# Performance work log

Measured on AMD Instinct MI355X. Metric: run time of the kernel, lower is better.

Reference implementation:

```python
import jax, jax.numpy as jnp
import numpy as np

N = 1024            # codeword length (power of 2)
NS = 10             # log2(N) butterfly stages
NUM_ITER = 10       # BP iterations
LLR_MAX = 19.3      # internal LLR clipping value
BS = 512            # batch size
FROZEN_POS = np.arange(64)
INFO_POS = np.setdiff1d(np.arange(N), FROZEN_POS)
K = len(INFO_POS)   # 960 information bits

# Precompute the per-stage butterfly gather patterns (static numpy indices).
_ind_range = np.arange(N // 2)
IND_1 = [(_ind_range * 2 - np.mod(_ind_range, 2 ** s)) for s in range(NS)]
IND_2 = [IND_1[s] + 2 ** s for s in range(NS)]
IND_INV = [np.argsort(np.concatenate([IND_1[s], IND_2[s]])) for s in range(NS)]


def _boxplus(x, y):
    # check-node update, matches tf: log(1+exp(x+y)) - log(exp(x)+exp(y))
    x = jnp.clip(x, -LLR_MAX, LLR_MAX)
    y = jnp.clip(y, -LLR_MAX, LLR_MAX)
    return jnp.log(1.0 + jnp.exp(x + y)) - jnp.log(jnp.exp(x) + jnp.exp(y))


def _bp_forward(llr_in):
    llr_ch = -llr_in  # logits -> internal llr sign convention (as in sionna's call)
    bs = llr_ch.shape[0]
    # a-priori right-messages: LLR_MAX at frozen positions, 0 elsewhere
    msg_r_in = jnp.zeros((1, N), jnp.float32).at[:, FROZEN_POS].set(LLR_MAX)
    msg_r_in = jnp.broadcast_to(msg_r_in, (bs, N))

    def one_iter(msg_l_prev, _):
        # msg_l_prev: [NS+1, bs, N]; slot s+1 feeds stage s of the next r-pass.
        # Initialized to zeros, which reproduces the ind_it==0 zero-init branch.
        # ---- right-going (check-node) pass, stages 0..NS-1 ----
        r_msgs = [msg_r_in]  # slot 0
        for s in range(NS):
            l_in = llr_ch if s == NS - 1 else msg_l_prev[s + 1]
            l1, l2 = l_in[:, IND_1[s]], l_in[:, IND_2[s]]
            r_in = r_msgs[s]
            r1, r2 = r_in[:, IND_1[s]], r_in[:, IND_2[s]]
            r1_out = _boxplus(r1, l2 + r2)
            r2_out = _boxplus(r1, l1) + r2
            r_out = jnp.concatenate([r1_out, r2_out], axis=1)[:, IND_INV[s]]
            r_msgs.append(r_out)
        # ---- left-going (bit-node) pass, stages NS-1..0 ----
        l_msgs = [None] * (NS + 1)
        l_msgs[NS] = llr_ch
        for s in range(NS - 1, -1, -1):
            l_in = l_msgs[s + 1]
            l1, l2 = l_in[:, IND_1[s]], l_in[:, IND_2[s]]
            r_in = r_msgs[s]
            r1, r2 = r_in[:, IND_1[s]], r_in[:, IND_2[s]]
            l1_out = _boxplus(l1, l2 + r2)
            l2_out = _boxplus(r1, l1) + l2
            l_msgs[s] = jnp.concatenate([l1_out, l2_out], axis=1)[:, IND_INV[s]]
        return jnp.stack(l_msgs, axis=0), None

    msg_l0 = jnp.zeros((NS + 1, bs, N), jnp.float32)
    msg_l, _ = jax.lax.scan(one_iter, msg_l0, None, length=NUM_ITER)
    u_hat = msg_l[0][:, INFO_POS]  # [bs, k] soft estimates (internal llr domain)
    return -u_hat                   # flip back to input logit convention


def setup_inputs() -> dict:
    key = jax.random.key(0)
    llr_ch = 2.0 * jax.random.normal(key, (BS, N), dtype=jnp.float32)
    return {"llr_ch": llr_ch}


def reference(llr_ch):
    return _bp_forward(llr_ch)
```

## Files before the change

### kernel.cpp

```cpp
#include <hip/hip_runtime.h>

#define BSZ 512
#define KOUT 960
#define EMAX 2.4092698e8f
#define EMIN 4.1506346e-9f

__device__ __forceinline__ float boxpE(float ex, float ey) {
    ex = fminf(fmaxf(ex, EMIN), EMAX);
    ey = fminf(fmaxf(ey, EMIN), EMAX);
    float num = __builtin_fmaf(ex, ey, 1.0f);
    float den = ex + ey;
    return num * __builtin_amdgcn_rcpf(den);
}

__global__ __launch_bounds__(512, 4) void polar_bp(const float* __restrict__ in,
                                                   float* __restrict__ out) {
    __shared__ float xbA[1024];
    __shared__ float xbB[1024];
    __shared__ float sL7[128];
    __shared__ float sL8[256];
    __shared__ float sL9[512];
    __shared__ float sR6[64];

    const int tid = threadIdx.x;
    const int batch = blockIdx.x;

    const float* inb = in + (size_t)batch * 1024;
    float llr0 = __expf(-inb[tid]);
    float llr1 = __expf(-inb[512 + tid]);

    float Ls[7];
    float Rs[6];
#pragma unroll
    for (int s = 0; s < 7; ++s) Ls[s] = 1.f;
#pragma unroll
    for (int s = 0; s < 6; ++s) Rs[s] = 1.f;

    if (tid < 128) sL7[tid] = 1.f;
    if (tid < 256) sL8[tid] = 1.f;
    sL9[tid] = 1.f;

    float Lc0 = 1.f, Lc1 = 1.f;

#pragma unroll 1
    for (int it = 0; it < 10; ++it) {
        if (tid < 64) {
            float r = EMAX;
#pragma unroll
            for (int s = 0; s <= 5; ++s) {
                float lp = __shfl_xor(Ls[s + 1], 1 << s, 64);
                float rp = __shfl_xor(r, 1 << s, 64);
                bool isB = (tid >> s) & 1;
                float x = isB ? rp : r;
                float y = isB ? lp : lp * rp;
                float c = boxpE(x, y);
                r = isB ? c * r : c;
                if (s <= 4) Rs[s + 1] = r;
            }
            sR6[tid] = r;
        }
        __syncthreads();

        float r6c = sR6[tid & 63];
        float r7c = boxpE(r6c, sL7[(tid & 127) ^ 64]);
        float r8c = boxpE(r7c, sL8[(tid & 255) ^ 128]);
        float r9c = boxpE(r8c, sL9[tid ^ 256]);

        float n0 = boxpE(llr0, llr1);
        Lc1 = boxpE(r9c, llr0) * llr1;
        Lc0 = n0;
        float Ls9r = n0;

        xbA[tid] = Lc0;
        xbA[512 + tid] = Lc1;
        __syncthreads();
        {
            float p0 = xbA[tid ^ 256];
            float p1 = xbA[512 + (tid ^ 256)];
            bool isB = tid >= 256;
            float x0 = isB ? r8c : Lc0;
            float c0 = boxpE(x0, p0);
            Lc0 = isB ? c0 * Lc0 : c0;
            float x1 = isB ? 1.f : Lc1;
            float c1 = boxpE(x1, p1);
            Lc1 = isB ? c1 * Lc1 : c1;
            sL9[tid] = Ls9r;
            if (!isB) sL8[tid] = Lc0;
        }

        xbB[tid] = Lc0;
        xbB[512 + tid] = Lc1;
        __syncthreads();
        {
            float p0 = xbB[tid ^ 128];
            float p1 = xbB[512 + (tid ^ 128)];
            bool isB = (tid >> 7) & 1;
            float r1 = (isB && tid < 256) ? r7c : 1.f;
            float x0 = isB ? r1 : Lc0;
            float c0 = boxpE(x0, p0);
            Lc0 = isB ? c0 * Lc0 : c0;
            float x1 = isB ? 1.f : Lc1;
            float c1 = boxpE(x1, p1);
            Lc1 = isB ? c1 * Lc1 : c1;
            if (tid < 128) sL7[tid] = Lc0;
        }

        xbA[tid] = Lc0;
        xbA[512 + tid] = Lc1;
        __syncthreads();
        {
            float p0 = xbA[tid ^ 64];
            float p1 = xbA[512 + (tid ^ 64)];
            bool isB = (tid >> 6) & 1;
            float r1 = (isB && tid < 128) ? r6c : 1.f;
            float x0 = isB ? r1 : Lc0;
            float c0 = boxpE(x0, p0);
            Lc0 = isB ? c0 * Lc0 : c0;
            float x1 = isB ? 1.f : Lc1;
            float c1 = boxpE(x1, p1);
            Lc1 = isB ? c1 * Lc1 : c1;
            Ls[6] = Lc0;
        }

#pragma unroll
        for (int s = 5; s >= 1; --s) {
            const int m = 1 << s;
            float rp = 1.f;
            if (tid < 64) rp = __shfl_xor(Rs[s], m, 64);
            float lp0 = __shfl_xor(Lc0, m, 64);
            float lp1 = __shfl_xor(Lc1, m, 64);
            bool isB = (tid >> s) & 1;
            float x0 = isB ? rp : Lc0;
            float y0 = isB ? lp0 : lp0 * rp;
            float c0 = boxpE(x0, y0);
            Lc0 = isB ? c0 * Lc0 : c0;
            float x1 = isB ? 1.f : Lc1;
            float c1 = boxpE(x1, lp1);
            Lc1 = isB ? c1 * Lc1 : c1;
            Ls[s] = Lc0;
        }
    }

    {
        float lp0 = __shfl_xor(Lc0, 1, 64);
        float lp1 = __shfl_xor(Lc1, 1, 64);
        bool odd = tid & 1;
        float e0 = odd ? Lc0 : boxpE(Lc0, lp0);
        float e1 = odd ? Lc1 : boxpE(Lc1, lp1);
        float o0 = -__logf(e0);
        float o1 = -__logf(e1);
        const size_t ob = (size_t)batch * KOUT;
        if (tid >= 64) out[ob + tid - 64] = o0;
        out[ob + 448 + tid] = o1;
    }
}

extern "C" void kernel_launch(void* const* d_in, const int* in_sizes, int n_in,
                              void* d_out, int out_size, void* d_ws, size_t ws_size,
                              hipStream_t stream) {
    const float* in = (const float*)d_in[0];
    float* out = (float*)d_out;
    polar_bp<<<BSZ, 512, 0, stream>>>(in, out);
}
```

Before: 73.27 us.

## Hoist iteration-invariant upper stages and run BP loop only in first wave

Recognizes that the upper-stage left messages (stages 6-9) do not depend on the iteration because the R inputs to the lower-half branches are constant. It precomputes them once before the loop, then runs the 10-iteration loop within only the first 64 threads using shuffles. The full 512-thread stages run once at the end. This removes most block-wide syncthreads and shared-memory traffic per iteration. Correctness relies on the frozen-set structure, where the first 64 positions are frozen.

```diff
diff --git a/kernel.cpp b/kernel.cpp
--- a/kernel.cpp
+++ b/kernel.cpp
@@ -9,42 +9,54 @@
     ex = fminf(fmaxf(ex, EMIN), EMAX);
     ey = fminf(fmaxf(ey, EMIN), EMAX);
     float num = __builtin_fmaf(ex, ey, 1.0f);
-    float den = ex + ey;
-    return num * __builtin_amdgcn_rcpf(den);
+    return num * __builtin_amdgcn_rcpf(ex + ey);
+}
+__device__ __forceinline__ float boxpE_nc(float ex, float ey) {
+    float num = __builtin_fmaf(ex, ey, 1.0f);
+    return num * __builtin_amdgcn_rcpf(ex + ey);
 }
 
 __global__ __launch_bounds__(512, 4) void polar_bp(const float* __restrict__ in,
                                                    float* __restrict__ out) {
     __shared__ float xbA[1024];
     __shared__ float xbB[1024];
+    __shared__ float xbC[128];
     __shared__ float sL7[128];
     __shared__ float sL8[256];
     __shared__ float sL9[512];
     __shared__ float sR6[64];
 
     const int tid = threadIdx.x;
-    const int batch = blockIdx.x;
-
-    const float* inb = in + (size_t)batch * 1024;
+    const float* inb = in + (size_t)blockIdx.x * 1024;
     float llr0 = __expf(-inb[tid]);
     float llr1 = __expf(-inb[512 + tid]);
 
-    float Ls[7];
+    float n0 = boxpE(llr0, llr1);
+    sL9[tid] = n0;
+    xbA[tid] = n0;
+    float Li8 = 0.f, Li7 = 0.f, Li6 = 0.f;
+    __syncthreads();
+    if (tid < 256) {
+        Li8 = boxpE_nc(n0, xbA[tid ^ 256]);
+        sL8[tid] = Li8;
+        xbB[tid] = Li8;
+    }
+    __syncthreads();
+    if (tid < 128) {
+        Li7 = boxpE_nc(Li8, xbB[tid ^ 128]);
+        sL7[tid] = Li7;
+        xbC[tid] = Li7;
+    }
+    __syncthreads();
+    if (tid < 64) Li6 = boxpE_nc(Li7, xbC[tid + 64]);
+
     float Rs[6];
+    if (tid < 64) {
+        float Ls[7];
 #pragma unroll
-    for (int s = 0; s < 7; ++s) Ls[s] = 1.f;
-#pragma unroll
-    for (int s = 0; s < 6; ++s) Rs[s] = 1.f;
-
-    if (tid < 128) sL7[tid] = 1.f;
-    if (tid < 256) sL8[tid] = 1.f;
-    sL9[tid] = 1.f;
-
-    float Lc0 = 1.f, Lc1 = 1.f;
-
+        for (int s = 0; s < 7; ++s) Ls[s] = 1.f;
 #pragma unroll 1
-    for (int it = 0; it < 10; ++it) {
-        if (tid < 64) {
+        for (int it = 0; it < 10; ++it) {
             float r = EMAX;
 #pragma unroll
             for (int s = 0; s <= 5; ++s) {
@@ -57,88 +69,95 @@
                 r = isB ? c * r : c;
                 if (s <= 4) Rs[s + 1] = r;
             }
-            sR6[tid] = r;
+            if (it == 9) { sR6[tid] = r; break; }
+            float Lc = Li6;
+#pragma unroll
+            for (int s = 5; s >= 1; --s) {
+                const int m = 1 << s;
+                float rp = __shfl_xor(Rs[s], m, 64);
+                float lp = __shfl_xor(Lc, m, 64);
+                bool isB = (tid >> s) & 1;
+                float x = isB ? rp : Lc;
+                float y = isB ? lp : lp * rp;
+                float c = boxpE(x, y);
+                Lc = isB ? c * Lc : c;
+                Ls[s] = Lc;
+            }
+            Ls[6] = Li6;
         }
-        __syncthreads();
+    }
+    __syncthreads();
 
-        float r6c = sR6[tid & 63];
-        float r7c = boxpE(r6c, sL7[(tid & 127) ^ 64]);
-        float r8c = boxpE(r7c, sL8[(tid & 255) ^ 128]);
-        float r9c = boxpE(r8c, sL9[tid ^ 256]);
+    float r6c = sR6[tid & 63];
+    float r7c = boxpE(r6c, sL7[(tid & 127) ^ 64]);
+    float r8c = boxpE(r7c, sL8[(tid & 255) ^ 128]);
+    float r9c = boxpE(r8c, sL9[tid ^ 256]);
 
-        float n0 = boxpE(llr0, llr1);
-        Lc1 = boxpE(r9c, llr0) * llr1;
-        Lc0 = n0;
-        float Ls9r = n0;
+    float Lc0 = n0;
+    float Lc1 = boxpE(r9c, llr0) * llr1;
 
-        xbA[tid] = Lc0;
-        xbA[512 + tid] = Lc1;
-        __syncthreads();
-        {
-            float p0 = xbA[tid ^ 256];
-            float p1 = xbA[512 + (tid ^ 256)];
-            bool isB = tid >= 256;
-            float x0 = isB ? r8c : Lc0;
-            float c0 = boxpE(x0, p0);
-            Lc0 = isB ? c0 * Lc0 : c0;
-            float x1 = isB ? 1.f : Lc1;
-            float c1 = boxpE(x1, p1);
-            Lc1 = isB ? c1 * Lc1 : c1;
-            sL9[tid] = Ls9r;
-            if (!isB) sL8[tid] = Lc0;
-        }
+    xbA[tid] = Lc0;
+    xbA[512 + tid] = Lc1;
+    __syncthreads();
+    {
+        float p0 = xbA[tid ^ 256];
+        float p1 = xbA[512 + (tid ^ 256)];
+        bool isB = tid >= 256;
+        float x0 = isB ? r8c : Lc0;
+        float c0 = boxpE(x0, p0);
+        Lc0 = isB ? c0 * Lc0 : c0;
+        float x1 = isB ? 1.f : Lc1;
+        float c1 = boxpE(x1, p1);
+        Lc1 = isB ? c1 * Lc1 : c1;
+    }
 
-        xbB[tid] = Lc0;
-        xbB[512 + tid] = Lc1;
-        __syncthreads();
-        {
-            float p0 = xbB[tid ^ 128];
-            float p1 = xbB[512 + (tid ^ 128)];
-            bool isB = (tid >> 7) & 1;
-            float r1 = (isB && tid < 256) ? r7c : 1.f;
-            float x0 = isB ? r1 : Lc0;
-            float c0 = boxpE(x0, p0);
-            Lc0 = isB ? c0 * Lc0 : c0;
-            float x1 = isB ? 1.f : Lc1;
-            float c1 = boxpE(x1, p1);
-            Lc1 = isB ? c1 * Lc1 : c1;
-            if (tid < 128) sL7[tid] = Lc0;
-        }
+    xbB[tid] = Lc0;
+    xbB[512 + tid] = Lc1;
+    __syncthreads();
+    {
+        float p0 = xbB[tid ^ 128];
+        float p1 = xbB[512 + (tid ^ 128)];
+        bool isB = (tid >> 7) & 1;
+        float r1 = (isB && tid < 256) ? r7c : 1.f;
+        float x0 = isB ? r1 : Lc0;
+        float c0 = boxpE(x0, p0);
+        Lc0 = isB ? c0 * Lc0 : c0;
+        float x1 = isB ? 1.f : Lc1;
+        float c1 = boxpE(x1, p1);
+        Lc1 = isB ? c1 * Lc1 : c1;
+    }
 
-        xbA[tid] = Lc0;
-        xbA[512 + tid] = Lc1;
-        __syncthreads();
-        {
-            float p0 = xbA[tid ^ 64];
-            float p1 = xbA[512 + (tid ^ 64)];
-            bool isB = (tid >> 6) & 1;
-            float r1 = (isB && tid < 128) ? r6c : 1.f;
-            float x0 = isB ? r1 : Lc0;
-            float c0 = boxpE(x0, p0);
-            Lc0 = isB ? c0 * Lc0 : c0;
-            float x1 = isB ? 1.f : Lc1;
-            float c1 = boxpE(x1, p1);
-            Lc1 = isB ? c1 * Lc1 : c1;
-            Ls[6] = Lc0;
-        }
+    xbA[tid] = Lc0;
+    xbA[512 + tid] = Lc1;
+    __syncthreads();
+    {
+        float p0 = xbA[tid ^ 64];
+        float p1 = xbA[512 + (tid ^ 64)];
+        bool isB = (tid >> 6) & 1;
+        float r1 = (isB && tid < 128) ? r6c : 1.f;
+        float x0 = isB ? r1 : Lc0;
+        float c0 = boxpE(x0, p0);
+        Lc0 = isB ? c0 * Lc0 : c0;
+        float x1 = isB ? 1.f : Lc1;
+        float c1 = boxpE(x1, p1);
+        Lc1 = isB ? c1 * Lc1 : c1;
+    }
 
 #pragma unroll
-        for (int s = 5; s >= 1; --s) {
-            const int m = 1 << s;
-            float rp = 1.f;
-            if (tid < 64) rp = __shfl_xor(Rs[s], m, 64);
-            float lp0 = __shfl_xor(Lc0, m, 64);
-            float lp1 = __shfl_xor(Lc1, m, 64);
-            bool isB = (tid >> s) & 1;
-            float x0 = isB ? rp : Lc0;
-            float y0 = isB ? lp0 : lp0 * rp;
-            float c0 = boxpE(x0, y0);
-            Lc0 = isB ? c0 * Lc0 : c0;
-            float x1 = isB ? 1.f : Lc1;
-            float c1 = boxpE(x1, lp1);
-            Lc1 = isB ? c1 * Lc1 : c1;
-            Ls[s] = Lc0;
-        }
+    for (int s = 5; s >= 1; --s) {
+        const int m = 1 << s;
+        float rp = 1.f;
+        if (tid < 64) rp = __shfl_xor(Rs[s], m, 64);
+        float lp0 = __shfl_xor(Lc0, m, 64);
+        float lp1 = __shfl_xor(Lc1, m, 64);
+        bool isB = (tid >> s) & 1;
+        float x0 = isB ? rp : Lc0;
+        float y0 = isB ? lp0 : lp0 * rp;
+        float c0 = boxpE(x0, y0);
+        Lc0 = isB ? c0 * Lc0 : c0;
+        float x1 = isB ? 1.f : Lc1;
+        float c1 = boxpE(x1, lp1);
+        Lc1 = isB ? c1 * Lc1 : c1;
     }
 
     {
@@ -149,7 +168,7 @@
         float e1 = odd ? Lc1 : boxpE(Lc1, lp1);
         float o0 = -__logf(e0);
         float o1 = -__logf(e1);
-        const size_t ob = (size_t)batch * KOUT;
+        const size_t ob = (size_t)blockIdx.x * KOUT;
         if (tid >= 64) out[ob + tid - 64] = o0;
         out[ob + 448 + tid] = o1;
     }
```

New measurement: 62.01 us. 15.4% less time.
